# Kernel tuning notes

Hardware: AMD Instinct MI355X
Metric: run time of the kernel (lower is better)

The kernel has to match this reference:

```python
import jax, jax.numpy as jnp
import numpy as np

IN_DIM = 512
HID = 1024
E = 16
TOPK = 2


def setup_inputs() -> dict:
    key = jax.random.key(0)
    ks = jax.random.split(key, 8)
    s = 0.02
    x = jax.random.normal(ks[0], (4, 2048, IN_DIM), dtype=jnp.float32)
    Wr = jax.random.normal(ks[1], (IN_DIM, E), dtype=jnp.float32) * s
    br = jnp.zeros((E,), dtype=jnp.float32)
    W1 = jax.random.normal(ks[2], (E, IN_DIM, HID), dtype=jnp.float32) * s
    b1 = jnp.zeros((E, HID), dtype=jnp.float32)
    W2 = jax.random.normal(ks[3], (E, HID, IN_DIM), dtype=jnp.float32) * s
    b2 = jnp.zeros((E, IN_DIM), dtype=jnp.float32)
    return {"x": x, "Wr": Wr, "br": br, "W1": W1, "b1": b1, "W2": W2, "b2": b2}


def reference(x, Wr, br, W1, b1, W2, b2):
    token_shape = x.shape[:-1]
    xf = x.reshape(-1, x.shape[-1])            # [T, D]
    T = xf.shape[0]

    # router (temperature = 1.0)
    logits = xf @ Wr + br                       # [T, E]
    probs = jax.nn.softmax(logits, axis=-1)
    topk_w, topk_idx = jax.lax.top_k(probs, TOPK)           # [T, K]
    topk_w = topk_w / jnp.maximum(topk_w.sum(-1, keepdims=True), 1e-9)

    # combine weights: [T, E], zero where not routed
    combine = jnp.zeros((T, E), dtype=xf.dtype).at[
        jnp.arange(T)[:, None], topk_idx].add(topk_w)

    # per-expert MLP (exact GELU, as torch nn.GELU default), weighted combine
    y = jnp.zeros_like(xf)
    for e in range(E):
        h = jax.nn.gelu(xf @ W1[e] + b1[e], approximate=False)  # [T, H]
        o = h @ W2[e] + b2[e]                                   # [T, D]
        y = y + combine[:, e:e + 1] * o

    # residual (in_dim == out_dim)
    y = xf + y
    return y.reshape(*token_shape, IN_DIM)
```

## Files before the change

### kernel.cpp

```cpp
#include <hip/hip_runtime.h>
#include <hip/hip_bf16.h>
#include <math.h>

#define IN_DIM 512
#define HID    1024
#define NE     16
#define T_TOK  8192
#define NPAIR  (T_TOK*2)

typedef __attribute__((ext_vector_type(8))) short bf16x8;
typedef __attribute__((ext_vector_type(4))) float f32x4;

__device__ __forceinline__ unsigned short f2b(float f){
  unsigned u = __float_as_uint(f);
  u += 0x7FFF + ((u >> 16) & 1);
  return (unsigned short)(u >> 16);
}
__device__ __forceinline__ float b2f(unsigned short u){
  return __uint_as_float(((unsigned)u) << 16);
}

__device__ __forceinline__ void barrier_lds_only(){
  asm volatile("s_waitcnt lgkmcnt(0)" ::: "memory");
  __builtin_amdgcn_s_barrier();
}

__global__ __launch_bounds__(256) void tconv_kernel(const float* __restrict__ in,
                                                    unsigned short* __restrict__ out,
                                                    int M, int N){
  __shared__ float tile[32][33];
  int e  = blockIdx.z;
  int m0 = blockIdx.y*32, n0 = blockIdx.x*32;
  const float* src = in + (size_t)e*M*N;
  unsigned short* dst = out + (size_t)e*M*N;
  int c = threadIdx.x & 31, r = threadIdx.x >> 5;
  #pragma unroll
  for (int i=0;i<4;i++)
    tile[r + i*8][c] = src[(size_t)(m0 + r + i*8)*N + n0 + c];
  __syncthreads();
  int tr  = threadIdx.x >> 3;
  int tc4 = (threadIdx.x & 7) * 4;
  ushort4 o;
  o.x = f2b(tile[tc4+0][tr]); o.y = f2b(tile[tc4+1][tr]);
  o.z = f2b(tile[tc4+2][tr]); o.w = f2b(tile[tc4+3][tr]);
  *(ushort4*)(&dst[(size_t)(n0 + tr)*M + m0 + tc4]) = o;
}

__global__ __launch_bounds__(256) void router_kernel(
    const float* __restrict__ x, const float* __restrict__ Wr, const float* __restrict__ br,
    unsigned short* __restrict__ xb, int* __restrict__ eid, float* __restrict__ pw)
{
  int wid = threadIdx.x >> 6, lane = threadIdx.x & 63;
  int t = blockIdx.x*4 + wid;
  const float4* xr4 = (const float4*)(x + (size_t)t*IN_DIM);
  ushort4*      xb4 = (ushort4*)(xb + (size_t)t*IN_DIM);

  float acc[NE];
  #pragma unroll
  for (int i=0;i<NE;i++) acc[i]=0.f;

  #pragma unroll
  for (int j=0;j<2;j++){
    int f = j*64 + lane;
    float4 v = xr4[f];
    ushort4 o; o.x=f2b(v.x); o.y=f2b(v.y); o.z=f2b(v.z); o.w=f2b(v.w);
    xb4[f] = o;
    const float4* wr4 = (const float4*)(Wr + (size_t)(f*4)*NE);
    const float* vv = (const float*)&v;
    #pragma unroll
    for (int rr=0; rr<4; rr++){
      float xv = vv[rr];
      #pragma unroll
      for (int q=0;q<4;q++){
        float4 w = wr4[rr*4+q];
        acc[q*4+0] += xv*w.x; acc[q*4+1] += xv*w.y;
        acc[q*4+2] += xv*w.z; acc[q*4+3] += xv*w.w;
      }
    }
  }
  #pragma unroll
  for (int off=32; off>=1; off>>=1){
    #pragma unroll
    for (int i=0;i<NE;i++) acc[i] += __shfl_xor(acc[i], off, 64);
  }
  if (lane==0){
    #pragma unroll
    for (int i=0;i<NE;i++) acc[i] += br[i];
    int e0=0; float l0=acc[0];
    #pragma unroll
    for (int i=1;i<NE;i++) if (acc[i] > l0){ l0=acc[i]; e0=i; }
    int e1=-1; float l1=-3.0e38f;
    #pragma unroll
    for (int i=0;i<NE;i++) if (i!=e0 && acc[i] > l1){ l1=acc[i]; e1=i; }
    float w0 = 1.f/(1.f + __expf(l1 - l0));
    float w1 = 1.f - w0;
    pw[t*2+0] = w0; pw[t*2+1] = w1;
    eid[t*2+0] = e0; eid[t*2+1] = e1;
  }
}

__global__ __launch_bounds__(1024) void bucket_kernel(const int* __restrict__ eid,
                                                      int* __restrict__ cnt,
                                                      int* __restrict__ bucket){
  int e = blockIdx.x;
  __shared__ int lbase;
  if (threadIdx.x == 0) lbase = 0;
  __syncthreads();
  int lane = threadIdx.x & 63, wid = threadIdx.x >> 6;
  int* be = bucket + e*T_TOK;
  for (int c = wid*64; c < NPAIR; c += 1024){
    int p = c + lane;
    bool ok = (eid[p] == e);
    unsigned long long m = __ballot(ok);
    int rank = __popcll(m & ((1ull << lane) - 1ull));
    int count = __popcll(m);
    int base = 0;
    if (lane == 0) base = atomicAdd(&lbase, count);
    base = __shfl(base, 0, 64);
    if (ok) be[base + rank] = p;
  }
  __syncthreads();
  if (threadIdx.x == 0) cnt[e] = lbase;
}

template<int KDIM, int NDIM, bool FIRST>
__global__ __launch_bounds__(256) void moe_gemm(
    const unsigned short* __restrict__ A,
    const unsigned short* __restrict__ Bm,
    const float* __restrict__ bias,
    const int* __restrict__ cnt,
    const int* __restrict__ bucket,
    const float* __restrict__ pw,
    unsigned short* __restrict__ hb,
    unsigned short* __restrict__ opb)
{
  constexpr int NS  = KDIM / 32;
  constexpr int NBT = NDIM / 128;

  int ntiles = 0;
  #pragma unroll
  for (int j=0;j<NE;j++) ntiles += ((cnt[j]+63)>>6)*NBT;

  __shared__ unsigned short As[2*64*32];
  __shared__ unsigned short Bs[2*128*32];

  int tid = threadIdx.x;
  int lane = tid & 63, wid = tid >> 6;
  int wm = (wid>>1)*32, wn = (wid&1)*64;
  int lr0 = tid >> 2;
  int c   = tid & 3;
  int sc  = (c ^ ((lr0 >> 1) & 3)) * 8;
  int wA  = lr0*32 + sc;
  int fr = lane & 15, fb = lane >> 4;
  int pf8 = (fb ^ ((fr >> 1) & 3)) * 8;
  int fq = (lane>>4)*4;

  for (int t = blockIdx.x; t < ntiles; t += gridDim.x){
    int e=0, tloc=0, ebase=0, ce=0, itl=1;
    {
      int cum=0, crow=0;
      #pragma unroll
      for (int j=0;j<NE;j++){
        int cj = cnt[j];
        int it = (cj+63)>>6;
        int tj = it * NBT;
        bool in = (t >= cum) & (t < cum+tj);
        if (in){ e=j; tloc=t-cum; ebase=crow; ce=cj; itl=it; }
        cum += tj; crow += cj;
      }
    }
    int i0 = (tloc % itl) * 64;
    int n0 = (tloc / itl) * 128;

    const int* buck = bucket + e*T_TOK;
    int posA = i0 + lr0;
    int arow;
    if (FIRST){
      int pair = (posA < ce) ? buck[posA] : buck[i0];
      arow = pair >> 1;
    } else {
      arow = ebase + posA;
      if (arow > NPAIR-1) arow = NPAIR-1;
    }
    const unsigned short* Ag = A + (size_t)arow*KDIM + c*8;
    const unsigned short* Bg = Bm + (size_t)e*NDIM*KDIM + (size_t)(n0 + lr0)*KDIM + c*8;

    f32x4 acc[2][4];
    #pragma unroll
    for (int a=0;a<2;a++)
      #pragma unroll
      for (int b=0;b<4;b++)
        #pragma unroll
        for (int j=0;j<4;j++) acc[a][b][j] = 0.f;

    float4 ar, br0, br1;
    ar  = *(const float4*)(Ag);
    br0 = *(const float4*)(Bg);
    br1 = *(const float4*)(Bg + (size_t)64*KDIM);
    *(float4*)(As + wA) = ar;
    *(float4*)(Bs + wA) = br0;
    *(float4*)(Bs + wA + 64*32) = br1;
    ar  = *(const float4*)(Ag + 32);
    br0 = *(const float4*)(Bg + 32);
    br1 = *(const float4*)(Bg + (size_t)64*KDIM + 32);
    barrier_lds_only();

    #pragma unroll 2
    for (int k = 0; k < NS; k++){
      const int cur = k & 1, nxt = cur ^ 1;
      float4 na, nb0, nb1;
      bool ld = (k + 2 < NS);
      if (ld){
        na  = *(const float4*)(Ag + (k+2)*32);
        nb0 = *(const float4*)(Bg + (k+2)*32);
        nb1 = *(const float4*)(Bg + (size_t)64*KDIM + (k+2)*32);
      }
      if (k + 1 < NS){
        *(float4*)(As + nxt*2048 + wA) = ar;
        *(float4*)(Bs + nxt*4096 + wA) = br0;
        *(float4*)(Bs + nxt*4096 + wA + 64*32) = br1;
      }
      if (ld){ ar = na; br0 = nb0; br1 = nb1; }

      const unsigned short* Ac = As + cur*2048;
      const unsigned short* Bc = Bs + cur*4096;
      bf16x8 af[2], bfr[4];
      #pragma unroll
      for (int s=0;s<2;s++) af[s]  = *(const bf16x8*)(Ac + (wm + s*16 + fr)*32 + pf8);
      #pragma unroll
      for (int u=0;u<4;u++) bfr[u] = *(const bf16x8*)(Bc + (wn + u*16 + fr)*32 + pf8);
      #pragma unroll
      for (int s=0;s<2;s++)
        #pragma unroll
        for (int u=0;u<4;u++)
          acc[s][u] = __builtin_amdgcn_mfma_f32_16x16x32_bf16(af[s], bfr[u], acc[s][u], 0,0,0);
      barrier_lds_only();
    }

    #pragma unroll
    for (int s=0;s<2;s++){
      #pragma unroll
      for (int i=0;i<4;i++){
        int row = wm + s*16 + fq + i;
        int pos = i0 + row;
        if (pos >= ce) continue;
        #pragma unroll
        for (int u=0;u<4;u++){
          int n = n0 + wn + u*16 + fr;
          float v = acc[s][u][i] + bias[e*NDIM + n];
          if (FIRST){
            float g = 0.5f*v*(1.f + erff(v*0.70710678118654752f));
            hb[(size_t)(ebase + pos)*NDIM + n] = f2b(g);
          } else {
            int pair = buck[pos];
            opb[(size_t)pair*NDIM + n] = f2b(pw[pair]*v);
          }
        }
      }
    }
  }
}

__global__ __launch_bounds__(256) void combine_kernel(const float* __restrict__ x,
                                                      const unsigned short* __restrict__ opb,
                                                      float* __restrict__ out){
  int i = blockIdx.x*256 + threadIdx.x;
  int t  = i >> 7;
  int c4 = i & 127;
  float4 v = ((const float4*)x)[i];
  ushort4 a = ((const ushort4*)opb)[(size_t)(2*t)*128 + c4];
  ushort4 b = ((const ushort4*)opb)[(size_t)(2*t+1)*128 + c4];
  v.x += b2f(a.x) + b2f(b.x);
  v.y += b2f(a.y) + b2f(b.y);
  v.z += b2f(a.z) + b2f(b.z);
  v.w += b2f(a.w) + b2f(b.w);
  ((float4*)out)[i] = v;
}

extern "C" void kernel_launch(void* const* d_in, const int* in_sizes, int n_in,
                              void* d_out, int out_size, void* d_ws, size_t ws_size,
                              hipStream_t stream)
{
  const float* x  = (const float*)d_in[0];
  const float* Wr = (const float*)d_in[1];
  const float* br = (const float*)d_in[2];
  const float* W1 = (const float*)d_in[3];
  const float* b1 = (const float*)d_in[4];
  const float* W2 = (const float*)d_in[5];
  const float* b2 = (const float*)d_in[6];
  float* out = (float*)d_out;
  char* ws = (char*)d_ws;

  int*            cnt    = (int*)(ws + 0);
  int*            bucket = (int*)(ws + 1024);
  float*          pw     = (float*)(ws + 525312);
  unsigned short* xb     = (unsigned short*)(ws + 590848);
  unsigned short* w1t    = (unsigned short*)(ws + 8979456);
  unsigned short* w2t    = (unsigned short*)(ws + 25756672);
  unsigned short* hb     = (unsigned short*)(ws + 42533888);
  int*            eid    = (int*)(ws + 42533888);
  unsigned short* opb    = w1t;

  router_kernel<<<T_TOK/4, 256, 0, stream>>>(x, Wr, br, xb, eid, pw);
  bucket_kernel<<<NE, 1024, 0, stream>>>(eid, cnt, bucket);
  tconv_kernel<<<dim3(HID/32, IN_DIM/32, NE), 256, 0, stream>>>(W1, w1t, IN_DIM, HID);
  tconv_kernel<<<dim3(IN_DIM/32, HID/32, NE), 256, 0, stream>>>(W2, w2t, HID, IN_DIM);
  moe_gemm<IN_DIM, HID, true ><<<1024, 256, 0, stream>>>(
      xb, w1t, b1, cnt, bucket, pw, hb, opb);
  moe_gemm<HID, IN_DIM, false><<<1024, 256, 0, stream>>>(
      hb, w2t, b2, cnt, bucket, pw, hb, opb);
  combine_kernel<<<(T_TOK*IN_DIM/4)/256, 256, 0, stream>>>(x, opb, out);
}
```

Before: 281.3 us.

## Fuse router and weight transposes into one launch, swizzle tiles, fast GELU

Merges the router kernel and both weight transpose/bf16-conversion kernels into a single launch partitioned by block index, with the transposes using 64x64 float4-loaded tiles and 8-wide stores. The grouped GEMM remaps the block-to-tile start order to interleave blocks across the tile space. The exact erf GELU is replaced with a tanh-style approximation computed via exp and fast division. This cuts launch overhead and special-function cost but changes GELU numerics slightly.

```diff
diff --git a/kernel.cpp b/kernel.cpp
--- a/kernel.cpp
+++ b/kernel.cpp
@@ -9,6 +9,7 @@
 #define NPAIR  (T_TOK*2)
 
 typedef __attribute__((ext_vector_type(8))) short bf16x8;
+typedef __attribute__((ext_vector_type(8))) unsigned short ushort8;
 typedef __attribute__((ext_vector_type(4))) float f32x4;
 
 __device__ __forceinline__ unsigned short f2b(float f){
@@ -25,77 +26,92 @@
   __builtin_amdgcn_s_barrier();
 }
 
-__global__ __launch_bounds__(256) void tconv_kernel(const float* __restrict__ in,
-                                                    unsigned short* __restrict__ out,
-                                                    int M, int N){
-  __shared__ float tile[32][33];
-  int e  = blockIdx.z;
-  int m0 = blockIdx.y*32, n0 = blockIdx.x*32;
-  const float* src = in + (size_t)e*M*N;
-  unsigned short* dst = out + (size_t)e*M*N;
-  int c = threadIdx.x & 31, r = threadIdx.x >> 5;
+__global__ __launch_bounds__(256) void fused_head(
+    const float* __restrict__ x, const float* __restrict__ Wr, const float* __restrict__ br,
+    unsigned short* __restrict__ xb, int* __restrict__ eid, float* __restrict__ pw,
+    const float* __restrict__ W1, unsigned short* __restrict__ O1,
+    const float* __restrict__ W2, unsigned short* __restrict__ O2)
+{
+  __shared__ float tile[64][65];
+  const int b = blockIdx.x;
+  const int tid = threadIdx.x;
+
+  if (b < 2048){
+    int wid = tid >> 6, lane = tid & 63;
+    int t = b*4 + wid;
+    const float4* xr4 = (const float4*)(x + (size_t)t*IN_DIM);
+    ushort4*      xb4 = (ushort4*)(xb + (size_t)t*IN_DIM);
+
+    float acc[NE];
+    #pragma unroll
+    for (int i=0;i<NE;i++) acc[i]=0.f;
+
+    #pragma unroll
+    for (int j=0;j<2;j++){
+      int f = j*64 + lane;
+      float4 v = xr4[f];
+      ushort4 o; o.x=f2b(v.x); o.y=f2b(v.y); o.z=f2b(v.z); o.w=f2b(v.w);
+      xb4[f] = o;
+      const float4* wr4 = (const float4*)(Wr + (size_t)(f*4)*NE);
+      const float* vv = (const float*)&v;
+      #pragma unroll
+      for (int rr=0; rr<4; rr++){
+        float xv = vv[rr];
+        #pragma unroll
+        for (int q=0;q<4;q++){
+          float4 w = wr4[rr*4+q];
+          acc[q*4+0] += xv*w.x; acc[q*4+1] += xv*w.y;
+          acc[q*4+2] += xv*w.z; acc[q*4+3] += xv*w.w;
+        }
+      }
+    }
+    #pragma unroll
+    for (int off=32; off>=1; off>>=1){
+      #pragma unroll
+      for (int i=0;i<NE;i++) acc[i] += __shfl_xor(acc[i], off, 64);
+    }
+    if (lane==0){
+      #pragma unroll
+      for (int i=0;i<NE;i++) acc[i] += br[i];
+      int e0=0; float l0=acc[0];
+      #pragma unroll
+      for (int i=1;i<NE;i++) if (acc[i] > l0){ l0=acc[i]; e0=i; }
+      int e1=-1; float l1=-3.0e38f;
+      #pragma unroll
+      for (int i=0;i<NE;i++) if (i!=e0 && acc[i] > l1){ l1=acc[i]; e1=i; }
+      float w0 = 1.f/(1.f + __expf(l1 - l0));
+      float w1 = 1.f - w0;
+      pw[t*2+0] = w0; pw[t*2+1] = w1;
+      eid[t*2+0] = e0; eid[t*2+1] = e1;
+    }
+    return;
+  }
+
+  const float* src; unsigned short* dst; int M, N, m0, n0;
+  if (b < 4096){
+    int b1 = b - 2048; M = IN_DIM; N = HID;
+    int e = b1 >> 7, r = b1 & 127;
+    n0 = (r & 15)*64; m0 = (r >> 4)*64;
+    src = W1 + (size_t)e*M*N; dst = O1 + (size_t)e*M*N;
+  } else {
+    int b2 = b - 4096; M = HID; N = IN_DIM;
+    int e = b2 >> 7, r = b2 & 127;
+    n0 = (r & 7)*64; m0 = (r >> 3)*64;
+    src = W2 + (size_t)e*M*N; dst = O2 + (size_t)e*M*N;
+  }
+  const int lr = tid >> 4, lc = (tid & 15)*4;
   #pragma unroll
   for (int i=0;i<4;i++)
-    tile[r + i*8][c] = src[(size_t)(m0 + r + i*8)*N + n0 + c];
+    *(float4*)&tile[lr + i*16][lc] = *(const float4*)&src[(size_t)(m0 + lr + i*16)*N + n0 + lc];
   __syncthreads();
-  int tr  = threadIdx.x >> 3;
-  int tc4 = (threadIdx.x & 7) * 4;
-  ushort4 o;
-  o.x = f2b(tile[tc4+0][tr]); o.y = f2b(tile[tc4+1][tr]);
-  o.z = f2b(tile[tc4+2][tr]); o.w = f2b(tile[tc4+3][tr]);
-  *(ushort4*)(&dst[(size_t)(n0 + tr)*M + m0 + tc4]) = o;
-}
-
-__global__ __launch_bounds__(256) void router_kernel(
-    const float* __restrict__ x, const float* __restrict__ Wr, const float* __restrict__ br,
-    unsigned short* __restrict__ xb, int* __restrict__ eid, float* __restrict__ pw)
-{
-  int wid = threadIdx.x >> 6, lane = threadIdx.x & 63;
-  int t = blockIdx.x*4 + wid;
-  const float4* xr4 = (const float4*)(x + (size_t)t*IN_DIM);
-  ushort4*      xb4 = (ushort4*)(xb + (size_t)t*IN_DIM);
-
-  float acc[NE];
+  const int nr = tid >> 3, mc = (tid & 7)*8;
   #pragma unroll
-  for (int i=0;i<NE;i++) acc[i]=0.f;
-
-  #pragma unroll
-  for (int j=0;j<2;j++){
-    int f = j*64 + lane;
-    float4 v = xr4[f];
-    ushort4 o; o.x=f2b(v.x); o.y=f2b(v.y); o.z=f2b(v.z); o.w=f2b(v.w);
-    xb4[f] = o;
-    const float4* wr4 = (const float4*)(Wr + (size_t)(f*4)*NE);
-    const float* vv = (const float*)&v;
-    #pragma unroll
-    for (int rr=0; rr<4; rr++){
-      float xv = vv[rr];
-      #pragma unroll
-      for (int q=0;q<4;q++){
-        float4 w = wr4[rr*4+q];
-        acc[q*4+0] += xv*w.x; acc[q*4+1] += xv*w.y;
-        acc[q*4+2] += xv*w.z; acc[q*4+3] += xv*w.w;
-      }
-    }
-  }
-  #pragma unroll
-  for (int off=32; off>=1; off>>=1){
-    #pragma unroll
-    for (int i=0;i<NE;i++) acc[i] += __shfl_xor(acc[i], off, 64);
-  }
-  if (lane==0){
-    #pragma unroll
-    for (int i=0;i<NE;i++) acc[i] += br[i];
-    int e0=0; float l0=acc[0];
-    #pragma unroll
-    for (int i=1;i<NE;i++) if (acc[i] > l0){ l0=acc[i]; e0=i; }
-    int e1=-1; float l1=-3.0e38f;
-    #pragma unroll
-    for (int i=0;i<NE;i++) if (i!=e0 && acc[i] > l1){ l1=acc[i]; e1=i; }
-    float w0 = 1.f/(1.f + __expf(l1 - l0));
-    float w1 = 1.f - w0;
-    pw[t*2+0] = w0; pw[t*2+1] = w1;
-    eid[t*2+0] = e0; eid[t*2+1] = e1;
+  for (int p=0;p<2;p++){
+    int n = nr + p*32;
+    ushort8 o;
+    #pragma unroll
+    for (int j=0;j<8;j++) o[j] = f2b(tile[mc+j][n]);
+    *(ushort8*)&dst[(size_t)(n0 + n)*M + m0 + mc] = o;
   }
 }
 
@@ -155,7 +171,8 @@
   int pf8 = (fb ^ ((fr >> 1) & 3)) * 8;
   int fq = (lane>>4)*4;
 
-  for (int t = blockIdx.x; t < ntiles; t += gridDim.x){
+  const int t0 = (blockIdx.x & 7)*(gridDim.x >> 3) + (blockIdx.x >> 3);
+  for (int t = t0; t < ntiles; t += gridDim.x){
     int e=0, tloc=0, ebase=0, ce=0, itl=1;
     {
       int cum=0, crow=0;
@@ -249,7 +266,8 @@
           int n = n0 + wn + u*16 + fr;
           float v = acc[s][u][i] + bias[e*NDIM + n];
           if (FIRST){
-            float g = 0.5f*v*(1.f + erff(v*0.70710678118654752f));
+            float z2 = v*(1.5957691216057308f + 0.0713548162726009f*v*v);
+            float g  = __fdividef(v, 1.f + __expf(-z2));
             hb[(size_t)(ebase + pos)*NDIM + n] = f2b(g);
           } else {
             int pair = buck[pos];
@@ -301,10 +319,8 @@
   int*            eid    = (int*)(ws + 42533888);
   unsigned short* opb    = w1t;
 
-  router_kernel<<<T_TOK/4, 256, 0, stream>>>(x, Wr, br, xb, eid, pw);
+  fused_head<<<6144, 256, 0, stream>>>(x, Wr, br, xb, eid, pw, W1, w1t, W2, w2t);
   bucket_kernel<<<NE, 1024, 0, stream>>>(eid, cnt, bucket);
-  tconv_kernel<<<dim3(HID/32, IN_DIM/32, NE), 256, 0, stream>>>(W1, w1t, IN_DIM, HID);
-  tconv_kernel<<<dim3(IN_DIM/32, HID/32, NE), 256, 0, stream>>>(W2, w2t, HID, IN_DIM);
   moe_gemm<IN_DIM, HID, true ><<<1024, 256, 0, stream>>>(
       xb, w1t, b1, cnt, bucket, pw, hb, opb);
   moe_gemm<HID, IN_DIM, false><<<1024, 256, 0, stream>>>(
```

Result: faster. 250.0 us (-11.1%).
